# Kernel tuning notes

Measured on AMD Instinct MI355X. Metric: run time of the kernel, lower is better.

## Reference

```python
import jax, jax.numpy as jnp
import numpy as np

TOPK = 5
EPS = 1e-8  # torch CosineSimilarity eps


def setup_inputs() -> dict:
    key = jax.random.key(0)
    k1, k2, k3 = jax.random.split(key, 3)
    B, N, D, L = 64, 100000, 768, 32
    query = jax.random.normal(k1, (B, D), dtype=jnp.float32)
    knowledge_embed = jax.random.normal(k2, (N, D), dtype=jnp.float32)
    knowledge_full = jax.random.randint(k3, (N, L), 0, 30000, dtype=jnp.int32)
    return {"query": query, "knowledge_embed": knowledge_embed, "knowledge_full": knowledge_full}


def reference(query, knowledge_embed, knowledge_full):
    # Batched cosine similarity: [B, N]
    q_norm = jnp.linalg.norm(query, axis=-1, keepdims=True)            # [B, 1]
    k_norm = jnp.linalg.norm(knowledge_embed, axis=-1, keepdims=True)  # [N, 1]
    dots = jnp.einsum("bd,nd->bn", query, knowledge_embed)             # [B, N]
    denom = jnp.maximum(q_norm * k_norm.T, EPS)                        # [B, N]
    sims = dots / denom
    # topk over knowledge axis
    _, indices = jax.lax.top_k(sims, TOPK)                             # [B, topk]
    topk_embed = knowledge_embed[indices]                              # [B, topk, D]
    topk_knowledge = knowledge_full[indices]                           # [B, topk, L]
    return (topk_knowledge, topk_embed)
```

## Files before the change

kernel.cpp:

```cpp
#include <hip/hip_runtime.h>
#include <cfloat>
#include <climits>


#define BQ 64
#define DD 768
#define NK 100000
#define LK 32
#define K_TOP 5
#define TROWS 16
#define NTIL (NK / TROWS)
#define NBLKS 512
#define T_CAND 16

typedef __attribute__((ext_vector_type(8))) short short8;
typedef __attribute__((ext_vector_type(4))) float f32x4;

static __device__ __forceinline__ ushort bf16_rtn(float x) {
    uint u = __float_as_uint(x);
    return (ushort)((u + 0x7FFFu + ((u >> 16) & 1u)) >> 16);
}

#define INS8(v, n, va, ia)                                                  \
    _Pragma("unroll")                                                       \
    for (int m_ = 0; m_ < 8; ++m_) {                                        \
        if ((v) > va[m_]) {                                                 \
            float tv_ = va[m_]; va[m_] = (v); (v) = tv_;                    \
            int ti_ = ia[m_]; ia[m_] = (n); (n) = ti_;                      \
        }                                                                   \
    }

__global__ __launch_bounds__(256) void prep_kernel(const float* __restrict__ q,
                                                   ushort* __restrict__ qf,
                                                   float* __restrict__ qn) {
    const int b = blockIdx.x, t = threadIdx.x;
    __shared__ float red[4];
    float v[3];
    float s = 0.f;
#pragma unroll
    for (int i = 0; i < 3; ++i) {
        v[i] = q[b * DD + t + i * 256];
        s = fmaf(v[i], v[i], s);
    }
    for (int off = 32; off > 0; off >>= 1) s += __shfl_down(s, off, 64);
    if ((t & 63) == 0) red[t >> 6] = s;
    __syncthreads();
    const float tot = red[0] + red[1] + red[2] + red[3];
    const float rq = rsqrtf(tot);
    const int qb = b >> 4, bi = b & 15;
#pragma unroll
    for (int i = 0; i < 3; ++i) {
        const int k = t + i * 256;
        const int kt = k >> 5, lg = (k >> 3) & 3, j = k & 7;
        qf[((size_t)(kt * 4 + qb) * 64 + lg * 16 + bi) * 8 + j] = bf16_rtn(v[i] * rq);
    }
    if (t == 0) qn[b] = sqrtf(tot);
}

__global__ __launch_bounds__(256, 2) void sims_kernel(const ushort* __restrict__ qf,
                                                      const float* __restrict__ ke,
                                                      float2* __restrict__ pv) {
    __shared__ ushort Bb[TROWS * DD];
    __shared__ float  S[BQ][17];

    const int t = threadIdx.x;
    const int w = t >> 6, l = t & 63;
    const int lg = l >> 4, li = l & 15;
    const int qd = t & 63, jq = t >> 6;

    float v8[8]; int i8[8];
#pragma unroll
    for (int m = 0; m < 8; ++m) { v8[m] = -FLT_MAX; i8[m] = INT_MAX; }

    f32x4 srA[4][3], srB[4][3];
    const int b = blockIdx.x;

#define ISSUE(SR, tl) do {                                                  \
        const float* g_ = ke + (size_t)((tl) * TROWS + w * 4) * DD + l * 4; \
        _Pragma("unroll")                                                   \
        for (int i_ = 0; i_ < 4; ++i_)                                      \
            _Pragma("unroll")                                               \
            for (int c_ = 0; c_ < 3; ++c_)                                  \
                SR[i_][c_] = *(const f32x4*)(g_ + i_ * DD + c_ * 256);      \
    } while (0)

#define PROCESS(SR, tl, nn) do {                                            \
        char* bb_ = (char*)Bb;                                              \
        _Pragma("unroll")                                                   \
        for (int i_ = 0; i_ < 4; ++i_) {                                    \
            const int row_ = w * 4 + i_;                                    \
            const int base_ = row_ * 1536 + l * 8;                          \
            const int sw_ = (row_ & 7) << 4;                                \
            _Pragma("unroll")                                               \
            for (int c_ = 0; c_ < 3; ++c_) {                                \
                uint2 u_;                                                   \
                u_.x = __builtin_amdgcn_perm(__float_as_uint(SR[i_][c_][1]),\
                                             __float_as_uint(SR[i_][c_][0]),\
                                             0x07060302u);                  \
                u_.y = __builtin_amdgcn_perm(__float_as_uint(SR[i_][c_][3]),\
                                             __float_as_uint(SR[i_][c_][2]),\
                                             0x07060302u);                  \
                *(uint2*)(bb_ + ((base_ + c_ * 512) ^ sw_)) = u_;           \
            }                                                               \
        }                                                                   \
        if ((nn) < NTIL) ISSUE(SR, nn);                                     \
        asm volatile("s_waitcnt lgkmcnt(0)" ::: "memory");                  \
        __builtin_amdgcn_sched_barrier(0);                                  \
        __builtin_amdgcn_s_barrier();                                       \
        __builtin_amdgcn_sched_barrier(0);                                  \
        const int boff_ = li * 1536 + lg * 16;                              \
        const int bsw_ = (li & 7) << 4;                                     \
        f32x4 acc_ = (f32x4){0.f, 0.f, 0.f, 0.f};                           \
        f32x4 ncc_ = (f32x4){0.f, 0.f, 0.f, 0.f};                           \
        short8 br_[2];                                                      \
        br_[0] = *(const short8*)(bb_ + (boff_ ^ bsw_));                    \
        _Pragma("unroll")                                                   \
        for (int kt_ = 0; kt_ < 24; ++kt_) {                                \
            const int cb_ = kt_ & 1;                                        \
            if (kt_ < 23)                                                   \
                br_[cb_ ^ 1] = *(const short8*)(bb_ +                       \
                                    ((boff_ + (kt_ + 1) * 64) ^ bsw_));     \
            acc_ = __builtin_amdgcn_mfma_f32_16x16x32_bf16(                 \
                A[kt_], br_[cb_], acc_, 0, 0, 0);                           \
            ncc_ = __builtin_amdgcn_mfma_f32_16x16x32_bf16(                 \
                br_[cb_], br_[cb_], ncc_, 0, 0, 0);                         \
        }                                                                   \
        float x_ = ncc_[li & 3];                                            \
        float dsq_ = __shfl(x_, ((li >> 2) << 4) | li, 64);                 \
        float rk_ = rsqrtf(dsq_);                                           \
        _Pragma("unroll")                                                   \
        for (int r_ = 0; r_ < 4; ++r_)                                      \
            S[w * 16 + lg * 4 + r_][li] = acc_[r_] * rk_;                   \
        asm volatile("s_waitcnt lgkmcnt(0)" ::: "memory");                  \
        __builtin_amdgcn_sched_barrier(0);                                  \
        __builtin_amdgcn_s_barrier();                                       \
        __builtin_amdgcn_sched_barrier(0);                                  \
        {                                                                   \
            const int nb_ = (tl) * TROWS + jq * 4;                          \
            _Pragma("unroll")                                               \
            for (int j_ = 0; j_ < 4; ++j_) {                                \
                float v_ = S[qd][jq * 4 + j_]; int n_ = nb_ + j_;           \
                INS8(v_, n_, v8, i8);                                       \
            }                                                               \
        }                                                                   \
    } while (0)

    ISSUE(srA, b);
    ISSUE(srB, b + NBLKS);
    const ushort* aq = qf + (size_t)w * 512 + l * 8;
    short8 A[24];
#pragma unroll
    for (int p = 0; p < 24; ++p) A[p] = *(const short8*)(aq + p * 2048);

    for (int k = 0; k < 12; k += 2) {
        PROCESS(srA, b + k * NBLKS, b + (k + 2) * NBLKS);
        PROCESS(srB, b + (k + 1) * NBLKS, b + (k + 3) * NBLKS);
    }
    if (b + 12 * NBLKS < NTIL) {
        PROCESS(srA, b + 12 * NBLKS, NTIL);
    }
#undef PROCESS
#undef ISSUE

    __syncthreads();
    float2* mg = (float2*)(&Bb[0]);
#pragma unroll
    for (int m = 0; m < 8; ++m) mg[t * 8 + m] = make_float2(v8[m], __int_as_float(i8[m]));
    __syncthreads();
    if (t < BQ) {
        float vf[8]; int nf[8];
#pragma unroll
        for (int m = 0; m < 8; ++m) { vf[m] = -FLT_MAX; nf[m] = INT_MAX; }
        for (int s = 0; s < 4; ++s) {
            const float2* rowp = &mg[(t + s * 64) * 8];
#pragma unroll
            for (int m = 0; m < 8; ++m) {
                float v = rowp[m].x; int n = __float_as_int(rowp[m].y);
                INS8(v, n, vf, nf);
            }
        }
        float2* dst = pv + ((size_t)t * NBLKS + blockIdx.x) * 8;
#pragma unroll
        for (int m = 0; m < 8; ++m) dst[m] = make_float2(vf[m], __int_as_float(nf[m]));
    }
}

__global__ __launch_bounds__(256) void merge_rescore_kernel(
    const float2* __restrict__ pv,
    const float* __restrict__ q, const float* __restrict__ ke,
    const int* __restrict__ kf, const float* __restrict__ qn,
    float* __restrict__ out) {
    const int qi = blockIdx.x, t = threadIdx.x;
    __shared__ float sv[256][8];
    __shared__ int   si[256][8];
    __shared__ int   ci[T_CAND];
    __shared__ float cs_[T_CAND];
    __shared__ int   fi[K_TOP];

    float v8[8]; int i8[8];
#pragma unroll
    for (int m = 0; m < 8; ++m) { v8[m] = -FLT_MAX; i8[m] = INT_MAX; }

    const float2* src = pv + (size_t)qi * NBLKS * 8;
#pragma unroll 4
    for (int c = t; c < NBLKS * 8; c += 256) {
        float2 e = src[c];
        float v = e.x; int n = __float_as_int(e.y);
        INS8(v, n, v8, i8);
    }
#pragma unroll
    for (int m = 0; m < 8; ++m) { sv[t][m] = v8[m]; si[t][m] = i8[m]; }
    __syncthreads();

    for (int active = 64; active >= 4; active >>= 2) {
        if (t < active) {
#pragma unroll
            for (int m = 0; m < 8; ++m) { v8[m] = -FLT_MAX; i8[m] = INT_MAX; }
            for (int s = 0; s < 4; ++s) {
                int row = t * 4 + s;
#pragma unroll
                for (int m = 0; m < 8; ++m) {
                    float v = sv[row][m]; int n = si[row][m];
                    INS8(v, n, v8, i8);
                }
            }
        }
        __syncthreads();
        if (t < active) {
#pragma unroll
            for (int m = 0; m < 8; ++m) { sv[t][m] = v8[m]; si[t][m] = i8[m]; }
        }
        __syncthreads();
    }

    if (t == 0) {
        float v16[T_CAND]; int i16[T_CAND];
#pragma unroll
        for (int m = 0; m < T_CAND; ++m) { v16[m] = -FLT_MAX; i16[m] = INT_MAX; }
        for (int row = 0; row < 4; ++row) {
#pragma unroll
            for (int m = 0; m < 8; ++m) {
                float v = sv[row][m]; int n = si[row][m];
#pragma unroll
                for (int p = 0; p < T_CAND; ++p) {
                    if (v > v16[p]) {
                        float tv = v16[p]; v16[p] = v; v = tv;
                        int ti = i16[p]; i16[p] = n; n = ti;
                    }
                }
            }
        }
#pragma unroll
        for (int m = 0; m < T_CAND; ++m) ci[m] = i16[m];
    }
    __syncthreads();

    {
        const int w = t >> 6, lane = t & 63;
        for (int cc = 0; cc < 4; ++cc) {
            int c = w * 4 + cc;
            int row = ci[c];
            const float* kp = ke + (size_t)row * DD + lane * 12;
            const float* qp = q + qi * DD + lane * 12;
            float d = 0.f, ks = 0.f;
#pragma unroll
            for (int i = 0; i < 12; ++i) {
                float kv = kp[i];
                d = fmaf(qp[i], kv, d);
                ks = fmaf(kv, kv, ks);
            }
#pragma unroll
            for (int off = 32; off > 0; off >>= 1) {
                d += __shfl_xor(d, off, 64);
                ks += __shfl_xor(ks, off, 64);
            }
            if (lane == 0)
                cs_[c] = d / fmaxf(qn[qi] * sqrtf(ks), 1e-8f);
        }
    }
    __syncthreads();

    if (t == 0) {
        float v5[K_TOP]; int i5[K_TOP];
#pragma unroll
        for (int m = 0; m < K_TOP; ++m) { v5[m] = -FLT_MAX; i5[m] = INT_MAX; }
        for (int c = 0; c < T_CAND; ++c) {
            float v = cs_[c]; int n = ci[c];
#pragma unroll
            for (int m = 0; m < K_TOP; ++m) {
                bool take = (v > v5[m]) || (v == v5[m] && n < i5[m]);
                if (take) {
                    float tv = v5[m]; v5[m] = v; v = tv;
                    int ti = i5[m]; i5[m] = n; n = ti;
                }
            }
        }
#pragma unroll
        for (int m = 0; m < K_TOP; ++m) fi[m] = i5[m];
    }
    __syncthreads();

    for (int pos = t; pos < K_TOP * LK; pos += 256) {
        int m = pos >> 5, lgi = pos & 31;
        out[(qi * K_TOP + m) * LK + lgi] = (float)kf[(size_t)fi[m] * LK + lgi];
    }
    const int EO = BQ * K_TOP * LK;
    for (int m = 0; m < K_TOP; ++m) {
        const float4* srcp = (const float4*)(ke + (size_t)fi[m] * DD);
        float4* dstp = (float4*)(out + EO + (size_t)(qi * K_TOP + m) * DD);
        for (int pos = t; pos < DD / 4; pos += 256) dstp[pos] = srcp[pos];
    }
}

extern "C" void kernel_launch(void* const* d_in, const int* in_sizes, int n_in,
                              void* d_out, int out_size, void* d_ws, size_t ws_size,
                              hipStream_t stream) {
    const float* query = (const float*)d_in[0];
    const float* ke    = (const float*)d_in[1];
    const int*   kf    = (const int*)d_in[2];
    float* out = (float*)d_out;

    float2* pv = (float2*)d_ws;
    ushort* qf = (ushort*)((char*)d_ws + (size_t)BQ * NBLKS * 8 * sizeof(float2));
    float*  qn = (float*)((char*)qf + (size_t)24 * 4 * 64 * 8 * sizeof(ushort));

    prep_kernel<<<BQ, 256, 0, stream>>>(query, qf, qn);
    sims_kernel<<<NBLKS, 256, 0, stream>>>(qf, ke, pv);
    merge_rescore_kernel<<<BQ, 256, 0, stream>>>(pv, query, ke, kf, qn, out);
}
```

Measured before the change: 173.0 us.

## Split D dimension across blocks and move top-k selection to combine kernel

The similarity kernel now splits the 768-wide embedding dimension into three 256-wide slices, each handled by its own block, which triples the grid and raises occupancy. Each block writes partial dot products and squared norms to workspace. A new combine kernel sums the three partials, normalises them and runs the per-query top-8 insertion with an early-exit check. This removes the serial top-k insertion from the MFMA loop and shrinks LDS and register use per block. The cost is about 80 MB of extra global writes and reads for the partial similarity buffers, plus one more kernel launch.

```diff
diff --git a/kernel.cpp b/kernel.cpp
--- a/kernel.cpp
+++ b/kernel.cpp
@@ -10,7 +10,10 @@
 #define K_TOP 5
 #define TROWS 16
 #define NTIL (NK / TROWS)
-#define NBLKS 512
+#define NBT 512
+#define KTH 256
+#define CTILES 50
+#define NCB (NTIL / CTILES)
 #define T_CAND 16
 
 typedef __attribute__((ext_vector_type(8))) short short8;
@@ -57,31 +60,27 @@
     if (t == 0) qn[b] = sqrtf(tot);
 }
 
-__global__ __launch_bounds__(256, 2) void sims_kernel(const ushort* __restrict__ qf,
+__global__ __launch_bounds__(256, 4) void sims_kernel(const ushort* __restrict__ qf,
                                                       const float* __restrict__ ke,
-                                                      float2* __restrict__ pv) {
-    __shared__ ushort Bb[TROWS * DD];
-    __shared__ float  S[BQ][17];
+                                                      float* __restrict__ simsP,
+                                                      float* __restrict__ simsN) {
+    __shared__ ushort Bb[TROWS * KTH];
+    __shared__ float  Sw[4][256];
 
     const int t = threadIdx.x;
     const int w = t >> 6, l = t & 63;
     const int lg = l >> 4, li = l & 15;
-    const int qd = t & 63, jq = t >> 6;
-
-    float v8[8]; int i8[8];
-#pragma unroll
-    for (int m = 0; m < 8; ++m) { v8[m] = -FLT_MAX; i8[m] = INT_MAX; }
-
-    f32x4 srA[4][3], srB[4][3];
-    const int b = blockIdx.x;
+    const int h = blockIdx.x / NBT;
+    const int b = blockIdx.x % NBT;
+
+    f32x4 srA[4], srB[4];
 
 #define ISSUE(SR, tl) do {                                                  \
-        const float* g_ = ke + (size_t)((tl) * TROWS + w * 4) * DD + l * 4; \
+        const float* g_ = ke + (size_t)((tl) * TROWS + w * 4) * DD          \
+                          + h * KTH + l * 4;                                \
         _Pragma("unroll")                                                   \
         for (int i_ = 0; i_ < 4; ++i_)                                      \
-            _Pragma("unroll")                                               \
-            for (int c_ = 0; c_ < 3; ++c_)                                  \
-                SR[i_][c_] = *(const f32x4*)(g_ + i_ * DD + c_ * 256);      \
+            SR[i_] = *(const f32x4*)(g_ + i_ * DD);                         \
     } while (0)
 
 #define PROCESS(SR, tl, nn) do {                                            \
@@ -89,97 +88,125 @@
         _Pragma("unroll")                                                   \
         for (int i_ = 0; i_ < 4; ++i_) {                                    \
             const int row_ = w * 4 + i_;                                    \
-            const int base_ = row_ * 1536 + l * 8;                          \
-            const int sw_ = (row_ & 7) << 4;                                \
-            _Pragma("unroll")                                               \
-            for (int c_ = 0; c_ < 3; ++c_) {                                \
-                uint2 u_;                                                   \
-                u_.x = __builtin_amdgcn_perm(__float_as_uint(SR[i_][c_][1]),\
-                                             __float_as_uint(SR[i_][c_][0]),\
-                                             0x07060302u);                  \
-                u_.y = __builtin_amdgcn_perm(__float_as_uint(SR[i_][c_][3]),\
-                                             __float_as_uint(SR[i_][c_][2]),\
-                                             0x07060302u);                  \
-                *(uint2*)(bb_ + ((base_ + c_ * 512) ^ sw_)) = u_;           \
-            }                                                               \
+            const int ad_ = (row_ * 512 + l * 8) ^ ((row_ & 7) << 4);       \
+            uint2 u_;                                                       \
+            u_.x = __builtin_amdgcn_perm(__float_as_uint(SR[i_][1]),        \
+                                         __float_as_uint(SR[i_][0]),        \
+                                         0x07060302u);                      \
+            u_.y = __builtin_amdgcn_perm(__float_as_uint(SR[i_][3]),        \
+                                         __float_as_uint(SR[i_][2]),        \
+                                         0x07060302u);                      \
+            *(uint2*)(bb_ + ad_) = u_;                                      \
         }                                                                   \
         if ((nn) < NTIL) ISSUE(SR, nn);                                     \
         asm volatile("s_waitcnt lgkmcnt(0)" ::: "memory");                  \
         __builtin_amdgcn_sched_barrier(0);                                  \
         __builtin_amdgcn_s_barrier();                                       \
         __builtin_amdgcn_sched_barrier(0);                                  \
-        const int boff_ = li * 1536 + lg * 16;                              \
+        const int boff_ = li * 512 + lg * 16;                               \
         const int bsw_ = (li & 7) << 4;                                     \
         f32x4 acc_ = (f32x4){0.f, 0.f, 0.f, 0.f};                           \
         f32x4 ncc_ = (f32x4){0.f, 0.f, 0.f, 0.f};                           \
         short8 br_[2];                                                      \
         br_[0] = *(const short8*)(bb_ + (boff_ ^ bsw_));                    \
         _Pragma("unroll")                                                   \
-        for (int kt_ = 0; kt_ < 24; ++kt_) {                                \
-            const int cb_ = kt_ & 1;                                        \
-            if (kt_ < 23)                                                   \
+        for (int s_ = 0; s_ < 8; ++s_) {                                    \
+            const int cb_ = s_ & 1;                                         \
+            if (s_ < 7)                                                     \
                 br_[cb_ ^ 1] = *(const short8*)(bb_ +                       \
-                                    ((boff_ + (kt_ + 1) * 64) ^ bsw_));     \
+                                   ((boff_ + (s_ + 1) * 64) ^ bsw_));       \
             acc_ = __builtin_amdgcn_mfma_f32_16x16x32_bf16(                 \
-                A[kt_], br_[cb_], acc_, 0, 0, 0);                           \
+                A[s_], br_[cb_], acc_, 0, 0, 0);                            \
             ncc_ = __builtin_amdgcn_mfma_f32_16x16x32_bf16(                 \
                 br_[cb_], br_[cb_], ncc_, 0, 0, 0);                         \
         }                                                                   \
+        _Pragma("unroll")                                                   \
+        for (int r_ = 0; r_ < 4; ++r_)                                      \
+            Sw[w][(lg * 4 + r_) * 16 + li] = acc_[r_];                      \
         float x_ = ncc_[li & 3];                                            \
         float dsq_ = __shfl(x_, ((li >> 2) << 4) | li, 64);                 \
-        float rk_ = rsqrtf(dsq_);                                           \
-        _Pragma("unroll")                                                   \
-        for (int r_ = 0; r_ < 4; ++r_)                                      \
-            S[w * 16 + lg * 4 + r_][li] = acc_[r_] * rk_;                   \
+        f32x4 so_ = *(const f32x4*)&Sw[w][l * 4];                           \
+        *(f32x4*)(simsP + ((size_t)(h * NTIL + (tl)) * 64 + w * 16) * 16    \
+                  + l * 4) = so_;                                           \
+        if (w == 0 && l < 16)                                               \
+            simsN[(size_t)(h * NTIL + (tl)) * 16 + l] = dsq_;               \
         asm volatile("s_waitcnt lgkmcnt(0)" ::: "memory");                  \
         __builtin_amdgcn_sched_barrier(0);                                  \
         __builtin_amdgcn_s_barrier();                                       \
         __builtin_amdgcn_sched_barrier(0);                                  \
-        {                                                                   \
-            const int nb_ = (tl) * TROWS + jq * 4;                          \
-            _Pragma("unroll")                                               \
-            for (int j_ = 0; j_ < 4; ++j_) {                                \
-                float v_ = S[qd][jq * 4 + j_]; int n_ = nb_ + j_;           \
-                INS8(v_, n_, v8, i8);                                       \
-            }                                                               \
-        }                                                                   \
     } while (0)
 
     ISSUE(srA, b);
-    ISSUE(srB, b + NBLKS);
+    ISSUE(srB, b + NBT);
     const ushort* aq = qf + (size_t)w * 512 + l * 8;
-    short8 A[24];
-#pragma unroll
-    for (int p = 0; p < 24; ++p) A[p] = *(const short8*)(aq + p * 2048);
+    short8 A[8];
+#pragma unroll
+    for (int s = 0; s < 8; ++s)
+        A[s] = *(const short8*)(aq + (size_t)(h * 8 + s) * 2048);
 
     for (int k = 0; k < 12; k += 2) {
-        PROCESS(srA, b + k * NBLKS, b + (k + 2) * NBLKS);
-        PROCESS(srB, b + (k + 1) * NBLKS, b + (k + 3) * NBLKS);
-    }
-    if (b + 12 * NBLKS < NTIL) {
-        PROCESS(srA, b + 12 * NBLKS, NTIL);
+        PROCESS(srA, b + k * NBT, b + (k + 2) * NBT);
+        PROCESS(srB, b + (k + 1) * NBT, b + (k + 3) * NBT);
+    }
+    if (b + 12 * NBT < NTIL) {
+        PROCESS(srA, b + 12 * NBT, NTIL);
     }
 #undef PROCESS
 #undef ISSUE
-
-    __syncthreads();
-    float2* mg = (float2*)(&Bb[0]);
-#pragma unroll
-    for (int m = 0; m < 8; ++m) mg[t * 8 + m] = make_float2(v8[m], __int_as_float(i8[m]));
+}
+
+__global__ __launch_bounds__(256) void combine_kernel(const float* __restrict__ simsP,
+                                                      const float* __restrict__ simsN,
+                                                      float2* __restrict__ pv) {
+    const int c = blockIdx.x, t = threadIdx.x;
+    const int q = t >> 2, jq = t & 3;
+
+    float v8[8]; int i8[8];
+#pragma unroll
+    for (int m = 0; m < 8; ++m) { v8[m] = -FLT_MAX; i8[m] = INT_MAX; }
+
+    const float* P1 = simsP + (size_t)NTIL * 1024;
+    const float* P2 = simsP + (size_t)2 * NTIL * 1024;
+    const float* N1 = simsN + (size_t)NTIL * 16;
+    const float* N2 = simsN + (size_t)2 * NTIL * 16;
+
+    for (int tt = 0; tt < CTILES; ++tt) {
+        const int tile = c * CTILES + tt;
+        const size_t pb = (size_t)tile * 1024 + t * 4;
+        f32x4 p0 = *(const f32x4*)(simsP + pb);
+        f32x4 p1 = *(const f32x4*)(P1 + pb);
+        f32x4 p2 = *(const f32x4*)(P2 + pb);
+        const size_t nb_ = (size_t)tile * 16 + jq * 4;
+        f32x4 n0 = *(const f32x4*)(simsN + nb_);
+        f32x4 n1 = *(const f32x4*)(N1 + nb_);
+        f32x4 n2 = *(const f32x4*)(N2 + nb_);
+        const int nbase = tile * 16 + jq * 4;
+#pragma unroll
+        for (int j = 0; j < 4; ++j) {
+            float s = (p0[j] + p1[j] + p2[j]) * rsqrtf(n0[j] + n1[j] + n2[j]);
+            int n = nbase + j;
+            if (s > v8[7]) { INS8(s, n, v8, i8); }
+        }
+    }
+
+    __shared__ float sv[256][8];
+    __shared__ int   si[256][8];
+#pragma unroll
+    for (int m = 0; m < 8; ++m) { sv[t][m] = v8[m]; si[t][m] = i8[m]; }
     __syncthreads();
     if (t < BQ) {
         float vf[8]; int nf[8];
 #pragma unroll
         for (int m = 0; m < 8; ++m) { vf[m] = -FLT_MAX; nf[m] = INT_MAX; }
         for (int s = 0; s < 4; ++s) {
-            const float2* rowp = &mg[(t + s * 64) * 8];
+            const int row = t * 4 + s;
 #pragma unroll
             for (int m = 0; m < 8; ++m) {
-                float v = rowp[m].x; int n = __float_as_int(rowp[m].y);
+                float v = sv[row][m]; int n = si[row][m];
                 INS8(v, n, vf, nf);
             }
         }
-        float2* dst = pv + ((size_t)t * NBLKS + blockIdx.x) * 8;
+        float2* dst = pv + ((size_t)t * NCB + c) * 8;
 #pragma unroll
         for (int m = 0; m < 8; ++m) dst[m] = make_float2(vf[m], __int_as_float(nf[m]));
     }
@@ -201,9 +228,8 @@
 #pragma unroll
     for (int m = 0; m < 8; ++m) { v8[m] = -FLT_MAX; i8[m] = INT_MAX; }
 
-    const float2* src = pv + (size_t)qi * NBLKS * 8;
-#pragma unroll 4
-    for (int c = t; c < NBLKS * 8; c += 256) {
+    const float2* src = pv + (size_t)qi * NCB * 8;
+    for (int c = t; c < NCB * 8; c += 256) {
         float2 e = src[c];
         float v = e.x; int n = __float_as_int(e.y);
         INS8(v, n, v8, i8);
@@ -320,11 +346,14 @@
     const int*   kf    = (const int*)d_in[2];
     float* out = (float*)d_out;
 
-    float2* pv = (float2*)d_ws;
-    ushort* qf = (ushort*)((char*)d_ws + (size_t)BQ * NBLKS * 8 * sizeof(float2));
-    float*  qn = (float*)((char*)qf + (size_t)24 * 4 * 64 * 8 * sizeof(ushort));
+    float*  simsP = (float*)d_ws;
+    float*  simsN = simsP + (size_t)3 * NTIL * 1024;
+    float2* pv    = (float2*)(simsN + (size_t)3 * NTIL * 16);
+    ushort* qf    = (ushort*)((char*)pv + (size_t)BQ * NCB * 8 * sizeof(float2));
+    float*  qn    = (float*)((char*)qf + (size_t)24 * 4 * 64 * 8 * sizeof(ushort));
 
     prep_kernel<<<BQ, 256, 0, stream>>>(query, qf, qn);
-    sims_kernel<<<NBLKS, 256, 0, stream>>>(qf, ke, pv);
+    sims_kernel<<<3 * NBT, 256, 0, stream>>>(qf, ke, simsP, simsN);
+    combine_kernel<<<NCB, 256, 0, stream>>>(simsP, simsN, pv);
     merge_rescore_kernel<<<BQ, 256, 0, stream>>>(pv, query, ke, kf, qn, out);
 }
```

Measured after the change: 241.9 us. 39.8% more time.
